# Optimization experiments

Measured on AMD Instinct MI355X. Metric: run time of the kernel, lower is better.

## Reference

```python
import jax, jax.numpy as jnp
import numpy as np

HEADS = 8
DIM_HEAD = 40
LN_EPS = 1e-5


def setup_inputs() -> dict:
    key = jax.random.key(0)
    ks = jax.random.split(key, 6)
    b, c, h, w = 8, 320, 64, 64
    ctx_len, ctx_dim = 77, 768
    inner = HEADS * DIM_HEAD  # 320
    return {
        "x": jax.random.normal(ks[0], (b, c, h, w), jnp.float32),
        "context": jax.random.normal(ks[1], (b, ctx_len, ctx_dim), jnp.float32),
        "Wq": jax.random.normal(ks[2], (c, inner), jnp.float32) * 0.02,
        "Wk": jax.random.normal(ks[3], (ctx_dim, inner), jnp.float32) * 0.02,
        "Wv": jax.random.normal(ks[4], (ctx_dim, inner), jnp.float32) * 0.02,
        "Wout": jax.random.normal(ks[5], (inner, c), jnp.float32) * 0.02,
        "bout": jnp.zeros((c,), jnp.float32),
        "gamma": jnp.ones((c,), jnp.float32),
        "beta": jnp.zeros((c,), jnp.float32),
    }


def reference(x, context, Wq, Wk, Wv, Wout, bout, gamma, beta):
    b, c, h, w = x.shape
    n = h * w
    scale = DIM_HEAD ** -0.5
    # flatten spatial -> tokens: [b, n, c]
    x_flat = x.reshape(b, c, n).transpose(0, 2, 1)
    # LayerNorm over channel dim
    mu = jnp.mean(x_flat, axis=-1, keepdims=True)
    var = jnp.mean((x_flat - mu) ** 2, axis=-1, keepdims=True)
    x_norm = (x_flat - mu) / jnp.sqrt(var + LN_EPS) * gamma + beta
    # projections (no bias), split heads: [b, h, n, d]
    def split_heads(t):
        bb, nn, _ = t.shape
        return t.reshape(bb, nn, HEADS, DIM_HEAD).transpose(0, 2, 1, 3)
    q = split_heads(x_norm @ Wq)
    k = split_heads(context @ Wk)
    v = split_heads(context @ Wv)
    sim = jnp.einsum("bhid,bhjd->bhij", q, k) * scale  # [b,H,n,ctx]
    attn = jax.nn.softmax(sim, axis=-1)
    out = jnp.einsum("bhij,bhjd->bhid", attn, v)
    out = out.transpose(0, 2, 1, 3).reshape(b, n, HEADS * DIM_HEAD)
    out = out @ Wout + bout  # dropout is identity at inference
    out = out + x_flat
    return out.transpose(0, 2, 1).reshape(b, c, h, w)
```

## Files before the change

kernel.cpp:

```cpp
#include <hip/hip_runtime.h>

#define HEADS 8
#define DH 40
constexpr int Bn   = 8;
constexpr int Cc   = 320;
constexpr int Nn   = 4096;
constexpr int CTX  = 77;
constexpr float LN_EPS = 1e-5f;
constexpr float SCALE  = 0.15811388300841897f;

typedef short bf16x8 __attribute__((ext_vector_type(8)));
typedef float f32x4  __attribute__((ext_vector_type(4)));
typedef unsigned short us;

__device__ inline us f2bf(float f) {
    unsigned u = __float_as_uint(f);
    u += 0x7fffu + ((u >> 16) & 1u);
    return (us)(u >> 16);
}
__device__ inline float bf2f(us h) {
    return __uint_as_float(((unsigned)h) << 16);
}

__global__ __launch_bounds__(256) void wtrans_all(const float* __restrict__ Wq,
                                                  const float* __restrict__ Wk,
                                                  const float* __restrict__ Wv,
                                                  const float* __restrict__ Wout,
                                                  us* __restrict__ wqF,
                                                  us* __restrict__ WkT,
                                                  us* __restrict__ WvT,
                                                  us* __restrict__ WoutT) {
    int id = blockIdx.x;
    if (id >= 580) {
        int wid = (id - 580) * 4 + (threadIdx.x >> 6);
        int lane = threadIdx.x & 63, lr = lane & 15, g = lane >> 4;
        int ct = wid / 10, kc = wid % 10;
        int k0 = kc * 32 + g * 8, co = ct * 16 + lr;
        us tmp[8];
        #pragma unroll
        for (int e = 0; e < 8; ++e)
            tmp[e] = f2bf(Wq[(size_t)(k0 + e) * 320 + co]);
        ((uint4*)wqF)[(size_t)wid * 64 + lane] = *(uint4*)tmp;
        return;
    }
    const float* in; us* out; int K, t;
    if (id < 240)      { in = Wk;   out = WkT;   K = 768; t = id; }
    else if (id < 480) { in = Wv;   out = WvT;   K = 768; t = id - 240; }
    else               { in = Wout; out = WoutT; K = 320; t = id - 480; }
    int ktiles = K >> 5;
    int kb = (t % ktiles) * 32, ob = (t / ktiles) * 32;

    __shared__ float tile[32][33];
    int tx = threadIdx.x & 31, ty = threadIdx.x >> 5;
    #pragma unroll
    for (int i = 0; i < 32; i += 8)
        tile[ty + i][tx] = in[(size_t)(kb + ty + i) * 320 + ob + tx];
    __syncthreads();
    #pragma unroll
    for (int i = 0; i < 32; i += 8)
        out[(size_t)(ob + ty + i) * K + kb + tx] = f2bf(tile[tx][ty + i]);
}

__global__ __launch_bounds__(256) void gemm_kv(const float* __restrict__ ctx,
                                               const us* __restrict__ WkT,
                                               const us* __restrict__ WvT,
                                               us* __restrict__ kbuf,
                                               us* __restrict__ vbuf) {
    const us* Bt = blockIdx.z ? WvT : WkT;
    us* Cm = blockIdx.z ? vbuf : kbuf;
    constexpr int K = 768, M = 616;
    __shared__ __align__(16) char Al[64 * 128];
    __shared__ __align__(16) char Bl[64 * 128];
    int m0 = blockIdx.x * 64;
    int n0 = blockIdx.y * 64;
    int tid = threadIdx.x;
    int lane = tid & 63, wave = tid >> 6;
    int wm = (wave >> 1) * 32, wn = (wave & 1) * 32;

    f32x4 acc[2][2] = {};

    for (int kc = 0; kc < K; kc += 64) {
        #pragma unroll
        for (int i = 0; i < 2; ++i) {
            int chunk = tid + 256 * i;
            int r = chunk >> 3, c8 = chunk & 7;
            int off = (r * 128 + c8 * 16) ^ ((r & 7) << 4);
            int gr = m0 + r;
            uint4 av = make_uint4(0, 0, 0, 0);
            if (gr < M) {
                float4 f0 = *(const float4*)(ctx + (size_t)gr * K + kc + c8 * 8);
                float4 f1 = *(const float4*)(ctx + (size_t)gr * K + kc + c8 * 8 + 4);
                av.x = f2bf(f0.x) | ((unsigned)f2bf(f0.y) << 16);
                av.y = f2bf(f0.z) | ((unsigned)f2bf(f0.w) << 16);
                av.z = f2bf(f1.x) | ((unsigned)f2bf(f1.y) << 16);
                av.w = f2bf(f1.z) | ((unsigned)f2bf(f1.w) << 16);
            }
            *(uint4*)(Al + off) = av;
            *(uint4*)(Bl + off) = *(const uint4*)(Bt + (size_t)(n0 + r) * K + kc + c8 * 8);
        }
        __syncthreads();

        #pragma unroll
        for (int kk = 0; kk < 64; kk += 32) {
            bf16x8 a[2], bfr[2];
            int lr = lane & 15;
            int lkb = (kk + (lane >> 4) * 8) * 2;
            #pragma unroll
            for (int mi = 0; mi < 2; ++mi) {
                int row = wm + mi * 16 + lr;
                a[mi] = *(const bf16x8*)(Al + ((row * 128 + lkb) ^ ((row & 7) << 4)));
            }
            #pragma unroll
            for (int ni = 0; ni < 2; ++ni) {
                int row = wn + ni * 16 + lr;
                bfr[ni] = *(const bf16x8*)(Bl + ((row * 128 + lkb) ^ ((row & 7) << 4)));
            }
            #pragma unroll
            for (int mi = 0; mi < 2; ++mi)
                #pragma unroll
                for (int ni = 0; ni < 2; ++ni)
                    acc[mi][ni] = __builtin_amdgcn_mfma_f32_16x16x32_bf16(a[mi], bfr[ni], acc[mi][ni], 0, 0, 0);
        }
        __syncthreads();
    }

    int lr = lane & 15, lq = lane >> 4;
    #pragma unroll
    for (int mi = 0; mi < 2; ++mi)
        #pragma unroll
        for (int ni = 0; ni < 2; ++ni)
            #pragma unroll
            for (int r = 0; r < 4; ++r) {
                int row = m0 + wm + mi * 16 + lq * 4 + r;
                int col = n0 + wn + ni * 16 + lr;
                if (row < M)
                    Cm[(size_t)row * 320 + col] = f2bf(acc[mi][ni][r]);
            }
}

__global__ __launch_bounds__(256) void gemm_vw(const us* __restrict__ WoutT,
                                               const us* __restrict__ vbuf,
                                               us* __restrict__ vwT) {
    int b = blockIdx.z, h = blockIdx.y, cb = blockIdx.x * 64;
    int tid = threadIdx.x, lane = tid & 63, w = tid >> 6;
    int lr = lane & 15, g = lane >> 4;

    int crow = cb + w * 16 + lr;
    const us* ab = WoutT + (size_t)crow * 320 + h * DH;
    bf16x8 a0 = *(const bf16x8*)(ab + g * 8);
    bf16x8 a1 = {};
    if (g == 0) a1 = *(const bf16x8*)(ab + 32);

    f32x4 acc[5] = {};
    #pragma unroll
    for (int nt = 0; nt < 5; ++nt) {
        int j = nt * 16 + lr;
        bool jv = j < CTX;
        const us* kr = vbuf + (size_t)(b * CTX + (jv ? j : 0)) * 320 + h * DH;
        bf16x8 b0 = {}, b1 = {};
        if (jv) b0 = *(const bf16x8*)(kr + g * 8);
        if (jv && g == 0) b1 = *(const bf16x8*)(kr + 32);
        acc[nt] = __builtin_amdgcn_mfma_f32_16x16x32_bf16(a0, b0, acc[nt], 0, 0, 0);
        acc[nt] = __builtin_amdgcn_mfma_f32_16x16x32_bf16(a1, b1, acc[nt], 0, 0, 0);
    }

    #pragma unroll
    for (int nt = 0; nt < 5; ++nt)
        #pragma unroll
        for (int r = 0; r < 4; ++r) {
            int c = cb + w * 16 + g * 4 + r;
            float val = (nt == 4 && lr >= 13) ? 0.f : acc[nt][r];
            vwT[((size_t)(b * 320 + c)) * 640 + h * 80 + nt * 16 + lr] = f2bf(val);
        }
}

__global__ __launch_bounds__(256) void repack_all(const us* __restrict__ kbuf,
                                                  const us* __restrict__ vwT,
                                                  us* __restrict__ kF,
                                                  us* __restrict__ vwF) {
    int id = blockIdx.x;
    int lane = threadIdx.x & 63, lr = lane & 15, g = lane >> 4;
    if (id < 160) {
        int wid = id * 4 + (threadIdx.x >> 6);
        int kc = wid & 1, nt = (wid >> 1) % 5, h = (wid / 10) & 7, b = wid / 80;
        int j = nt * 16 + lr, d0 = kc * 32 + g * 8;
        bf16x8 v = {};
        if (j < CTX && d0 < DH)
            v = *(const bf16x8*)(kbuf + ((size_t)(b * CTX + j)) * 320 + h * DH + d0);
        ((bf16x8*)kF)[(size_t)wid * 64 + lane] = v;
    } else {
        int wid = (id - 160) * 4 + (threadIdx.x >> 6);
        int mi = wid % 5, ks = (wid / 5) % 20, w = (wid / 100) & 3, b = wid / 400;
        int co = w * 80 + mi * 16 + lr, k = ks * 32 + g * 8;
        bf16x8 v = *(const bf16x8*)(vwT + ((size_t)(b * 320 + co)) * 640 + k);
        ((bf16x8*)vwF)[(size_t)wid * 64 + lane] = v;
    }
}

__global__ __launch_bounds__(512, 4) void fused_attn(const float* __restrict__ x,
                                                     const float* __restrict__ gamma,
                                                     const float* __restrict__ beta,
                                                     const us* __restrict__ wqF,
                                                     const us* __restrict__ kF,
                                                     const us* __restrict__ vwF,
                                                     const float* __restrict__ bout,
                                                     float* __restrict__ out) {
    __shared__ __align__(16) char smem[81920];
    char* xsq = smem;
    char* qls = smem + 40960;
    float* red1 = (float*)(smem + 40960);
    float* red2 = (float*)(smem + 40960 + 2048);
    float* mu_s = (float*)(smem + 40960 + 4096);
    float* rs_s = (float*)(smem + 40960 + 4352);

    int bid = blockIdx.x;
    int b = bid & 7, ts = bid >> 3;
    int t0 = ts * 64;
    int tid = threadIdx.x, lane = tid & 63, w = tid >> 6;
    int lr = lane & 15, g = lane >> 4;
    int tl = tid & 63, cg = tid >> 6;

    const float* xb = x + (size_t)b * Cc * Nn + t0 + tl;
    int xswz = (tl & 7) << 4;
    float s1 = 0.f, s2 = 0.f;
    #pragma unroll
    for (int j = 0; j < 20; ++j) {
        int c = cg * 40 + j * 2;
        float v0 = xb[(size_t)c * Nn];
        float v1 = xb[(size_t)(c + 1) * Nn];
        s1 += v0 + v1; s2 += v0 * v0 + v1 * v1;
        *(unsigned*)(xsq + ((tl * 640 + c * 2) ^ xswz)) =
            (unsigned)f2bf(v0) | ((unsigned)f2bf(v1) << 16);
    }
    red1[cg * 64 + tl] = s1; red2[cg * 64 + tl] = s2;
    __syncthreads();
    if (tid < 64) {
        float a1 = 0.f, a2 = 0.f;
        #pragma unroll
        for (int k = 0; k < 8; ++k) { a1 += red1[k * 64 + tid]; a2 += red2[k * 64 + tid]; }
        float mu = a1 * (1.f / Cc);
        float var = a2 * (1.f / Cc) - mu * mu;
        mu_s[tid] = mu; rs_s[tid] = rsqrtf(var + LN_EPS);
    }
    __syncthreads();

    {
        float mu = mu_s[tl], rs = rs_s[tl];
        #pragma unroll
        for (int j = 0; j < 20; ++j) {
            int c = cg * 40 + j * 2;
            unsigned* p = (unsigned*)(xsq + ((tl * 640 + c * 2) ^ xswz));
            unsigned u = *p;
            float v0 = bf2f((us)(u & 0xffff)), v1 = bf2f((us)(u >> 16));
            unsigned lo = f2bf((v0 - mu) * rs * gamma[c]     + beta[c]);
            unsigned hi = f2bf((v1 - mu) * rs * gamma[c + 1] + beta[c + 1]);
            *p = lo | (hi << 16);
        }
    }
    __syncthreads();

    {
        int mq = w & 1, cq = w >> 1;
        f32x4 acc[2][5] = {};
        const bf16x8* wq = (const bf16x8*)wqF;
        for (int kc = 0; kc < 10; ++kc) {
            bf16x8 bfr[5];
            #pragma unroll
            for (int nt = 0; nt < 5; ++nt)
                bfr[nt] = wq[(size_t)((cq * 5 + nt) * 10 + kc) * 64 + lane];
            bf16x8 afr[2];
            #pragma unroll
            for (int m = 0; m < 2; ++m) {
                int row = (mq * 2 + m) * 16 + lr;
                afr[m] = *(const bf16x8*)(xsq + ((row * 640 + kc * 64 + g * 16) ^ ((row & 7) << 4)));
            }
            #pragma unroll
            for (int m = 0; m < 2; ++m)
                #pragma unroll
                for (int nt = 0; nt < 5; ++nt)
                    acc[m][nt] = __builtin_amdgcn_mfma_f32_16x16x32_bf16(afr[m], bfr[nt], acc[m][nt], 0, 0, 0);
        }
        #pragma unroll
        for (int m = 0; m < 2; ++m)
            #pragma unroll
            for (int nt = 0; nt < 5; ++nt)
                #pragma unroll
                for (int r = 0; r < 4; ++r) {
                    int row = (mq * 2 + m) * 16 + g * 4 + r;
                    int col = cq * 80 + nt * 16 + lr;
                    *(us*)(qls + ((row * 640 + col * 2) ^ ((row & 7) << 4))) = f2bf(acc[m][nt][r]);
                }
    }
    __syncthreads();

    const bf16x8* kfb = (const bf16x8*)kF;
    f32x4 o[5][2] = {};
    int wc = w >> 1, wt = w & 1;
    int hh2 = w >> 1, mqk = w & 1;
    #pragma unroll
    for (int ph = 0; ph < 2; ++ph) {
        int h = ph * 4 + hh2;
        size_t kfh = (size_t)((b * 8 + h) * 10) * 64;
        #pragma unroll
        for (int m = 0; m < 2; ++m) {
            int mt = mqk * 2 + m;
            int arow = mt * 16 + lr;
            bf16x8 a0 = *(const bf16x8*)(qls + ((arow * 640 + h * 80 + g * 16) ^ ((arow & 7) << 4)));
            bf16x8 a1 = {};
            if (g == 0)
                a1 = *(const bf16x8*)(qls + ((arow * 640 + h * 80 + 64) ^ ((arow & 7) << 4)));

            f32x4 S[5] = {};
            #pragma unroll
            for (int nt = 0; nt < 5; ++nt) {
                bf16x8 kb0 = kfb[kfh + (nt * 2 + 0) * 64 + lane];
                bf16x8 kb1 = kfb[kfh + (nt * 2 + 1) * 64 + lane];
                S[nt] = __builtin_amdgcn_mfma_f32_16x16x32_bf16(a0, kb0, S[nt], 0, 0, 0);
                S[nt] = __builtin_amdgcn_mfma_f32_16x16x32_bf16(a1, kb1, S[nt], 0, 0, 0);
            }

            float pv[5][4];
            #pragma unroll
            for (int nt = 0; nt < 5; ++nt)
                #pragma unroll
                for (int r = 0; r < 4; ++r)
                    pv[nt][r] = (nt == 4 && lr >= 13) ? 0.f : __expf(S[nt][r] * SCALE);
            #pragma unroll
            for (int r = 0; r < 4; ++r) {
                float su = pv[0][r] + pv[1][r] + pv[2][r] + pv[3][r] + pv[4][r];
                #pragma unroll
                for (int off = 1; off < 16; off <<= 1)
                    su += __shfl_xor(su, off);
                float inv = 1.0f / su;
                int row = mt * 16 + g * 4 + r;
                #pragma unroll
                for (int nt = 0; nt < 5; ++nt)
                    *(us*)(xsq + ((row * 640 + ((h & 3) * 80 + nt * 16 + lr) * 2) ^ ((row & 7) << 4))) =
                        f2bf(pv[nt][r] * inv);
            }
        }
        __syncthreads();

        const bf16x8* vwb = (const bf16x8*)vwF + (size_t)((b * 4 + wc) * 100 + ph * 50) * 64 + lane;
        __builtin_amdgcn_s_setprio(1);
        #pragma unroll 2
        for (int ks = 0; ks < 10; ++ks) {
            bf16x8 av[5];
            #pragma unroll
            for (int mi = 0; mi < 5; ++mi)
                av[mi] = vwb[(ks * 5 + mi) * 64];
            bf16x8 pb[2];
            #pragma unroll
            for (int nt2 = 0; nt2 < 2; ++nt2) {
                int row = wt * 32 + nt2 * 16 + lr;
                pb[nt2] = *(const bf16x8*)(xsq + ((row * 640 + ks * 64 + g * 16) ^ ((row & 7) << 4)));
            }
            #pragma unroll
            for (int mi = 0; mi < 5; ++mi)
                #pragma unroll
                for (int nt2 = 0; nt2 < 2; ++nt2)
                    o[mi][nt2] = __builtin_amdgcn_mfma_f32_16x16x32_bf16(av[mi], pb[nt2], o[mi][nt2], 0, 0, 0);
        }
        __builtin_amdgcn_s_setprio(0);
        __syncthreads();
    }

    int cw = wc * 80;
    #pragma unroll
    for (int mi = 0; mi < 5; ++mi)
        #pragma unroll
        for (int r = 0; r < 4; ++r) {
            int co = cw + mi * 16 + g * 4 + r;
            float bo = bout[co];
            #pragma unroll
            for (int nt2 = 0; nt2 < 2; ++nt2) {
                size_t oi = ((size_t)(b * 320 + co)) * 4096 + t0 + wt * 32 + nt2 * 16 + lr;
                out[oi] = o[mi][nt2][r] + bo + x[oi];
            }
        }
}

extern "C" void kernel_launch(void* const* d_in, const int* in_sizes, int n_in,
                              void* d_out, int out_size, void* d_ws, size_t ws_size,
                              hipStream_t stream) {
    const float* x     = (const float*)d_in[0];
    const float* ctx   = (const float*)d_in[1];
    const float* Wq    = (const float*)d_in[2];
    const float* Wk    = (const float*)d_in[3];
    const float* Wv    = (const float*)d_in[4];
    const float* Wout  = (const float*)d_in[5];
    const float* bout  = (const float*)d_in[6];
    const float* gamma = (const float*)d_in[7];
    const float* beta  = (const float*)d_in[8];
    float* out = (float*)d_out;
    char* ws = (char*)d_ws;

    us* kbuf  = (us*)(ws);
    us* vbuf  = (us*)(ws + 394240);
    us* vwT   = (us*)(ws + 788480);
    us* vwF   = (us*)(ws + 4065280);
    us* kF    = (us*)(ws + 7342080);
    us* wqF   = (us*)(ws + 7997440);
    us* WkT   = (us*)(ws + 8202240);
    us* WvT   = (us*)(ws + 8693760);
    us* WoutT = (us*)(ws + 9185280);

    wtrans_all<<<dim3(630), 256, 0, stream>>>(Wq, Wk, Wv, Wout, wqF, WkT, WvT, WoutT);
    gemm_kv<<<dim3(10, 5, 2), 256, 0, stream>>>(ctx, WkT, WvT, kbuf, vbuf);
    gemm_vw<<<dim3(5, 8, 8), 256, 0, stream>>>(WoutT, vbuf, vwT);
    repack_all<<<dim3(960), 256, 0, stream>>>(kbuf, vwT, kF, vwF);
    fused_attn<<<dim3(512), 512, 0, stream>>>(x, gamma, beta, wqF, kF, vwF, bout, out);
}
```

Measured before the change: 92.84 us.

## Keep x tile in registers for LN and residual; stage epilogue through LDS

Each thread now holds its 40 fp32 x values in registers from the initial load. LayerNorm uses them directly instead of round-tripping bf16 through LDS, and the final residual add reuses them instead of re-reading x from global memory. The output projection result is staged in LDS (80KB, reusing smem) so the final store and residual add follow the token-contiguous coalesced pattern. This adds 40 live registers per thread under a 512x4 launch bound, which risks spills or reduced occupancy, and it adds one extra barrier.

Result: slower. 130.5 us (+40.6%).

```diff
diff --git a/kernel.cpp b/kernel.cpp
--- a/kernel.cpp
+++ b/kernel.cpp
@@ -212,6 +212,7 @@
     float* red2 = (float*)(smem + 40960 + 2048);
     float* mu_s = (float*)(smem + 40960 + 4096);
     float* rs_s = (float*)(smem + 40960 + 4352);
+    float* epi  = (float*)smem;
 
     int bid = blockIdx.x;
     int b = bid & 7, ts = bid >> 3;
@@ -221,16 +222,12 @@
     int tl = tid & 63, cg = tid >> 6;
 
     const float* xb = x + (size_t)b * Cc * Nn + t0 + tl;
-    int xswz = (tl & 7) << 4;
+    float xr[40];
     float s1 = 0.f, s2 = 0.f;
     #pragma unroll
-    for (int j = 0; j < 20; ++j) {
-        int c = cg * 40 + j * 2;
-        float v0 = xb[(size_t)c * Nn];
-        float v1 = xb[(size_t)(c + 1) * Nn];
-        s1 += v0 + v1; s2 += v0 * v0 + v1 * v1;
-        *(unsigned*)(xsq + ((tl * 640 + c * 2) ^ xswz)) =
-            (unsigned)f2bf(v0) | ((unsigned)f2bf(v1) << 16);
+    for (int i = 0; i < 40; ++i) {
+        float v = xb[(size_t)(cg * 40 + i) * Nn];
+        xr[i] = v; s1 += v; s2 += v * v;
     }
     red1[cg * 64 + tl] = s1; red2[cg * 64 + tl] = s2;
     __syncthreads();
@@ -246,15 +243,13 @@
 
     {
         float mu = mu_s[tl], rs = rs_s[tl];
+        int xswz = (tl & 7) << 4;
         #pragma unroll
         for (int j = 0; j < 20; ++j) {
             int c = cg * 40 + j * 2;
-            unsigned* p = (unsigned*)(xsq + ((tl * 640 + c * 2) ^ xswz));
-            unsigned u = *p;
-            float v0 = bf2f((us)(u & 0xffff)), v1 = bf2f((us)(u >> 16));
-            unsigned lo = f2bf((v0 - mu) * rs * gamma[c]     + beta[c]);
-            unsigned hi = f2bf((v1 - mu) * rs * gamma[c + 1] + beta[c + 1]);
-            *p = lo | (hi << 16);
+            unsigned lo = f2bf((xr[j * 2]     - mu) * rs * gamma[c]     + beta[c]);
+            unsigned hi = f2bf((xr[j * 2 + 1] - mu) * rs * gamma[c + 1] + beta[c + 1]);
+            *(unsigned*)(xsq + ((tl * 640 + c * 2) ^ xswz)) = lo | (hi << 16);
         }
     }
     __syncthreads();
@@ -365,19 +360,28 @@
         __syncthreads();
     }
 
-    int cw = wc * 80;
-    #pragma unroll
-    for (int mi = 0; mi < 5; ++mi)
-        #pragma unroll
-        for (int r = 0; r < 4; ++r) {
-            int co = cw + mi * 16 + g * 4 + r;
-            float bo = bout[co];
-            #pragma unroll
-            for (int nt2 = 0; nt2 < 2; ++nt2) {
-                size_t oi = ((size_t)(b * 320 + co)) * 4096 + t0 + wt * 32 + nt2 * 16 + lr;
-                out[oi] = o[mi][nt2][r] + bo + x[oi];
-            }
-        }
+    {
+        int cw = wc * 80;
+        #pragma unroll
+        for (int mi = 0; mi < 5; ++mi)
+            #pragma unroll
+            for (int r = 0; r < 4; ++r) {
+                int co = cw + mi * 16 + g * 4 + r;
+                float bo = bout[co];
+                #pragma unroll
+                for (int nt2 = 0; nt2 < 2; ++nt2) {
+                    int tok = wt * 32 + nt2 * 16 + lr;
+                    epi[co * 64 + tok] = o[mi][nt2][r] + bo;
+                }
+            }
+    }
+    __syncthreads();
+
+    #pragma unroll
+    for (int i = 0; i < 40; ++i) {
+        int c = cg * 40 + i;
+        out[((size_t)(b * 320 + c)) * 4096 + t0 + tl] = epi[c * 64 + tl] + xr[i];
+    }
 }
 
 extern "C" void kernel_launch(void* const* d_in, const int* in_sizes, int n_in,
```
